# Kernel tuning notes

Hardware: AMD Instinct MI355X
Metric: run time of the kernel (lower is better)

Reference implementation:

```python
import jax, jax.numpy as jnp
import numpy as np
from jax import lax

# ConvTranspose2d(stride=1, padding=p) == conv with spatially-flipped, in/out-swapped
# weight and padding k-1-p per side. Here k=3, p=1 -> conv padding (1,1).
K = 3
P = 1
_CONV_PAD = K - 1 - P  # = 1

def _rconv(a, w):
    # a: [N,C,H,Wf] real, w: [O,I,kH,kW]
    return lax.conv_general_dilated(
        a, w, window_strides=(1, 1),
        padding=[(_CONV_PAD, _CONV_PAD), (_CONV_PAD, _CONV_PAD)],
        dimension_numbers=("NCHW", "OIHW", "NCHW"))


def setup_inputs() -> dict:
    key = jax.random.key(0)
    k1, k2, k3, k4, k5 = jax.random.split(key, 5)
    N, C_IN, C_OUT, H, W = 8, 16, 16, 512, 512
    x = jax.random.normal(k1, (N, C_IN, H, W), dtype=jnp.float32)
    # torch ConvTranspose2d weight layout: (in, out, kH, kW), complex64 split into re/im
    scale = 1.0 / np.sqrt(C_IN * K * K)
    w_real = jax.random.normal(k2, (C_IN, C_OUT, K, K), dtype=jnp.float32) * scale
    w_imag = jax.random.normal(k3, (C_IN, C_OUT, K, K), dtype=jnp.float32) * scale
    b_real = jax.random.normal(k4, (C_OUT,), dtype=jnp.float32) * scale
    b_imag = jax.random.normal(k5, (C_OUT,), dtype=jnp.float32) * scale
    return {"x": x, "w_real": w_real, "w_imag": w_imag, "b_real": b_real, "b_imag": b_imag}


def reference(x, w_real, w_imag, b_real, b_imag):
    # rfftn over last two dims (norm='backward')
    X = jnp.fft.rfftn(x, axes=(-2, -1), norm="backward")  # [N,C,H,W//2+1] complex64
    Xr, Xi = jnp.real(X), jnp.imag(X)
    # convert transpose-conv weight to equivalent conv weight: flip spatial, swap in/out
    wr = jnp.transpose(jnp.flip(w_real, axis=(-2, -1)), (1, 0, 2, 3))
    wi = jnp.transpose(jnp.flip(w_imag, axis=(-2, -1)), (1, 0, 2, 3))
    # complex conv via real/imag decomposition
    Yr = _rconv(Xr, wr) - _rconv(Xi, wi) + b_real[:, None, None]
    Yi = _rconv(Xr, wi) + _rconv(Xi, wr) + b_imag[:, None, None]
    Y = lax.complex(Yr, Yi)
    # irfftn with no explicit s: last dim -> 2*(Wf-1) = W
    return jnp.fft.irfftn(Y, axes=(-2, -1), norm="backward")
```

## Files before the change

### kernel.cpp

```cpp
#include <hip/hip_runtime.h>
#include <math.h>

#define PI_F 3.14159265358979323846f

#define FI(i) ((i) + ((i) >> 4))
#define CSTRIDE 544

__device__ inline float2 cmulf(float2 a, float2 b) {
    return make_float2(a.x * b.x - a.y * b.y, a.x * b.y + a.y * b.x);
}
__device__ inline float2 cadd(float2 a, float2 b) { return make_float2(a.x + b.x, a.y + b.y); }
__device__ inline float2 csub(float2 a, float2 b) { return make_float2(a.x - b.x, a.y - b.y); }

__device__ inline void cmac(float2& a, float2 w, float2 v) {
    a.x = fmaf(w.x, v.x, a.x);
    a.x = fmaf(-w.y, v.y, a.x);
    a.y = fmaf(w.x, v.y, a.y);
    a.y = fmaf(w.y, v.x, a.y);
}

__device__ inline int xcd_remap(int bid, int q) {
    return (bid & 7) * q + (bid >> 3);
}

__device__ inline void build_tbl128(float2* tbl, int tid) {
    if (tid < 128) {
        float ang = -2.0f * PI_F * (float)tid * (1.0f / 512.0f);
        tbl[tid] = make_float2(cosf(ang), sinf(ang));
    }
}

template <int NCOLS>
__device__ inline float2* fft512_r4(float2* a, float2* b, const float2* tbl, int tid, bool inv) {
    const int bf = tid & 127;
    const int cp = tid >> 7;
#pragma unroll
    for (int st = 0; st < 4; ++st) {
        const int slog = 2 * st;
        const int s = 1 << slog;
        const int p = bf >> slog;
        const int q = bf & (s - 1);
        float2 w1 = tbl[p << slog];
        if (inv) w1.y = -w1.y;
        const float2 w2 = cmulf(w1, w1);
        const float2 w3 = cmulf(w2, w1);
        const int i0 = bf;
        const int ob = q + (p << (slog + 2));
#pragma unroll
        for (int t = 0; t < NCOLS / 2; ++t) {
            const int cc = cp + 2 * t;
            const float2* ac = a + cc * CSTRIDE;
            float2* bc = b + cc * CSTRIDE;
            float2 A = ac[FI(i0)];
            float2 B = ac[FI(i0 + 128)];
            float2 C = ac[FI(i0 + 256)];
            float2 D = ac[FI(i0 + 384)];
            float2 apc = cadd(A, C), amc = csub(A, C);
            float2 bpd = cadd(B, D), bmd = csub(B, D);
            float2 jb = make_float2(-bmd.y, bmd.x);
            if (inv) { jb.x = -jb.x; jb.y = -jb.y; }
            bc[FI(ob)]           = cadd(apc, bpd);
            bc[FI(ob + s)]       = cmulf(csub(amc, jb), w1);
            bc[FI(ob + 2 * s)]   = cmulf(csub(apc, bpd), w2);
            bc[FI(ob + 3 * s)]   = cmulf(cadd(amc, jb), w3);
        }
        __syncthreads();
        float2* tmp = a; a = b; b = tmp;
    }
    {
#pragma unroll
        for (int cc = 0; cc < NCOLS; ++cc) {
            const float2* ac = a + cc * CSTRIDE;
            float2* bc = b + cc * CSTRIDE;
            float2 A = ac[FI(tid)];
            float2 B = ac[FI(tid + 256)];
            bc[FI(tid)]       = cadd(A, B);
            bc[FI(tid + 256)] = csub(A, B);
        }
        __syncthreads();
        float2* tmp = a; a = b; b = tmp;
    }
    return a;
}

__global__ __launch_bounds__(256) void k_row_rfft(const float* __restrict__ x,
                                                  float2* __restrict__ G) {
    __shared__ float2 b0[4 * CSTRIDE], b1[4 * CSTRIDE], tbl[128];
    int tid = threadIdx.x;
    int nc = blockIdx.x >> 7;
    int h0 = (blockIdx.x & 127) * 4;
    build_tbl128(tbl, tid);
    const float4* xr = (const float4*)(x + ((size_t)nc * 512 + h0) * 512);
#pragma unroll
    for (int j = 0; j < 2; ++j) {
        int t4 = tid + 256 * j;
        float4 v = xr[t4];
        int e = t4 * 4;
        int k = e >> 9, i = e & 511;
        float2* dst = b0 + k * CSTRIDE + FI(i);
        dst[0] = make_float2(v.x, 0.0f);
        dst[1] = make_float2(v.y, 0.0f);
        dst[2] = make_float2(v.z, 0.0f);
        dst[3] = make_float2(v.w, 0.0f);
    }
    __syncthreads();
    float2* res = fft512_r4<4>(b0, b1, tbl, tid, false);
#pragma unroll
    for (int k = 0; k < 4; ++k) {
        float2* g = G + ((size_t)(nc * 512 + h0 + k)) * 257;
        g[tid] = res[k * CSTRIDE + FI(tid)];
        if (tid == 0) g[256] = res[k * CSTRIDE + FI(256)];
    }
}

__global__ __launch_bounds__(256) void k_col_fft(const float2* __restrict__ G,
                                                 float2* __restrict__ XT) {
    __shared__ float2 b0[4 * CSTRIDE], b1[4 * CSTRIDE], tbl[128];
    int tid = threadIdx.x;
    int l = xcd_remap(blockIdx.x, 1040);
    int nc = l / 65;
    int v0 = (l % 65) * 4;
    build_tbl128(tbl, tid);
#pragma unroll
    for (int i = 0; i < 8; ++i) {
        int e = tid + 256 * i;
        int k = e & 3, h = e >> 2;
        int v = v0 + k;
        float2 val = make_float2(0.0f, 0.0f);
        if (v < 257) val = G[((size_t)nc * 512 + h) * 257 + v];
        b0[k * CSTRIDE + FI(h)] = val;
    }
    __syncthreads();
    float2* res = fft512_r4<4>(b0, b1, tbl, tid, false);
#pragma unroll
    for (int k = 0; k < 4; ++k) {
        int v = v0 + k;
        if (v < 257) {
            float2* dst = XT + ((size_t)nc * 257 + v) * 512;
            dst[tid]       = res[k * CSTRIDE + FI(tid)];
            dst[tid + 256] = res[k * CSTRIDE + FI(tid + 256)];
        }
    }
}

__global__ __launch_bounds__(256, 4) void k_conv(const float2* __restrict__ XT,
                                                 float2* __restrict__ YT,
                                                 const float* __restrict__ wr,
                                                 const float* __restrict__ wi,
                                                 const float* __restrict__ br,
                                                 const float* __restrict__ bi) {
    __shared__ float2 Xs[16 * 4 * 66];
    int tid = threadIdx.x;
    int bid = blockIdx.x;
    int ut = bid & 7;
    int rest = bid >> 3;
    int vt = rest % 129;
    int n = rest / 129;
    int u0 = ut * 64;
    int v0 = vt * 2;

    for (int l = tid; l < 4224; l += 256) {
        int c = l / 264;
        int rem = l - c * 264;
        int dvr = rem / 66;
        int uu = rem - dvr * 66;
        int vg = v0 - 1 + dvr;
        int ug = u0 - 1 + uu;
        float2 val = make_float2(0.0f, 0.0f);
        if (vg >= 0 && vg < 257 && ug >= 0 && ug < 512)
            val = XT[(((size_t)n * 16 + c) * 257 + vg) * 512 + ug];
        Xs[l] = val;
    }
    __syncthreads();

    int lane = tid & 63;
    int wv = __builtin_amdgcn_readfirstlane(tid >> 6);
    int o0 = wv * 4;

    float2 acc[2][4];
#pragma unroll
    for (int oo = 0; oo < 4; ++oo) {
        float2 bv = make_float2(br[o0 + oo], bi[o0 + oo]);
        acc[0][oo] = bv;
        acc[1][oo] = bv;
    }

    for (int c = 0; c < 16; ++c) {
        float2 xv[4][3];
#pragma unroll
        for (int dvr = 0; dvr < 4; ++dvr) {
            const float2* row = &Xs[(c * 4 + dvr) * 66];
            xv[dvr][0] = row[lane];
            xv[dvr][1] = row[lane + 1];
            xv[dvr][2] = row[lane + 2];
        }
#pragma unroll
        for (int oo = 0; oo < 4; ++oo) {
            const float* wrp = wr + ((size_t)(c * 16 + o0 + oo)) * 9;
            const float* wip = wi + ((size_t)(c * 16 + o0 + oo)) * 9;
            float wre[9], wim[9];
#pragma unroll
            for (int t = 0; t < 9; ++t) { wre[t] = wrp[t]; wim[t] = wip[t]; }
#pragma unroll
            for (int kw = 0; kw < 3; ++kw) {
#pragma unroll
                for (int kh = 0; kh < 3; ++kh) {
                    int t = kh * 3 + kw;
                    int xj = 2 - kh;
                    float2 w = make_float2(wre[t], wim[t]);
                    cmac(acc[0][oo], w, xv[2 - kw][xj]);
                    cmac(acc[1][oo], w, xv[3 - kw][xj]);
                }
            }
        }
    }

#pragma unroll
    for (int oo = 0; oo < 4; ++oo) {
#pragma unroll
        for (int vv = 0; vv < 2; ++vv) {
            int v = v0 + vv;
            if (v < 257)
                YT[(((size_t)n * 16 + o0 + oo) * 257 + v) * 512 + u0 + lane] =
                    acc[vv][oo];
        }
    }
}

__global__ __launch_bounds__(256) void k_col_ifft(const float2* __restrict__ YT,
                                                  float2* __restrict__ ZT) {
    __shared__ float2 b0[4 * CSTRIDE], b1[4 * CSTRIDE], tbl[128];
    int tid = threadIdx.x;
    int no = blockIdx.x / 65;
    int v0 = (blockIdx.x % 65) * 4;
    build_tbl128(tbl, tid);
#pragma unroll
    for (int k = 0; k < 4; ++k) {
        int v = v0 + k;
        const float2* src = YT + ((size_t)no * 257 + (v < 257 ? v : 256)) * 512;
        b0[k * CSTRIDE + FI(tid)]       = src[tid];
        b0[k * CSTRIDE + FI(tid + 256)] = src[tid + 256];
    }
    __syncthreads();
    float2* res = fft512_r4<4>(b0, b1, tbl, tid, true);
    const float sc = 1.0f / 512.0f;
#pragma unroll
    for (int k = 0; k < 4; ++k) {
        int v = v0 + k;
        if (v < 257) {
            float2* dst = ZT + ((size_t)no * 257 + v) * 512;
            float2 r0 = res[k * CSTRIDE + FI(tid)];
            float2 r1 = res[k * CSTRIDE + FI(tid + 256)];
            dst[tid]       = make_float2(r0.x * sc, r0.y * sc);
            dst[tid + 256] = make_float2(r1.x * sc, r1.y * sc);
        }
    }
}

__global__ __launch_bounds__(256) void k_row_irfft(const float2* __restrict__ ZT,
                                                   float* __restrict__ out) {
    __shared__ float2 b0[4 * CSTRIDE], b1[4 * CSTRIDE], tbl[128];
    int tid = threadIdx.x;
    int l = xcd_remap(blockIdx.x, 2048);
    int no = l >> 7;
    int h0 = (l & 127) * 4;
    build_tbl128(tbl, tid);
#pragma unroll
    for (int i = 0; i < 5; ++i) {
        int e = tid + 256 * i;
        if (e < 1028) {
            int k = e & 3, vv = e >> 2;
            float2 val = ZT[((size_t)no * 257 + vv) * 512 + h0 + k];
            if (vv == 0 || vv == 256) val.y = 0.0f;
            b0[k * CSTRIDE + FI(vv)] = val;
        }
    }
    __syncthreads();
#pragma unroll
    for (int i = 0; i < 4; ++i) {
        int e = tid + 256 * i;
        if (e < 1020) {
            int k = e & 3, vv = 257 + (e >> 2);
            float2 s = b0[k * CSTRIDE + FI(512 - vv)];
            b0[k * CSTRIDE + FI(vv)] = make_float2(s.x, -s.y);
        }
    }
    __syncthreads();
    float2* res = fft512_r4<4>(b0, b1, tbl, tid, true);
    const float sc = 1.0f / 512.0f;
#pragma unroll
    for (int k = 0; k < 4; ++k) {
        float* dst = out + ((size_t)no * 512 + h0 + k) * 512;
        dst[tid]       = res[k * CSTRIDE + FI(tid)].x * sc;
        dst[tid + 256] = res[k * CSTRIDE + FI(tid + 256)].x * sc;
    }
}

extern "C" void kernel_launch(void* const* d_in, const int* in_sizes, int n_in,
                              void* d_out, int out_size, void* d_ws, size_t ws_size,
                              hipStream_t stream) {
    const float* x  = (const float*)d_in[0];
    const float* wr = (const float*)d_in[1];
    const float* wi = (const float*)d_in[2];
    const float* br = (const float*)d_in[3];
    const float* bi = (const float*)d_in[4];
    float* out = (float*)d_out;

    const size_t bufElems = (size_t)128 * 257 * 512;
    float2* A = (float2*)d_ws;
    float2* B = A + bufElems;

    k_row_rfft<<<128 * 128, 256, 0, stream>>>(x, A);
    k_col_fft<<<128 * 65, 256, 0, stream>>>(A, B);
    k_conv<<<8 * 129 * 8, 256, 0, stream>>>(B, A, wr, wi, br, bi);
    k_col_ifft<<<128 * 65, 256, 0, stream>>>(A, B);
    k_row_irfft<<<128 * 128, 256, 0, stream>>>(B, out);
}
```

Measured before the change: 674.6 us.

## Replace block-wide radix-4 FFT with per-wave register radix-8 FFT

Replaces the shared-memory radix-4 FFT, which used five block-wide barriers and a twiddle table, with a per-wavefront 512-point FFT. Each lane holds 8 values in registers and runs three radix-8 stages with two LDS transposes between them. Wave-local fences replace __syncthreads, and twiddles come from sincosf instead of a table. This is meant to cut barrier stalls and LDS traffic. In exchange it adds transcendental math and more register pressure, and the column kernels now do strided, uncoalesced global loads per lane. The Hermitian extension in the irfft row kernel now reads ZT directly instead of mirroring in LDS.

New measurement: 697.5 us. +3.4%, slower.

```diff
diff --git a/kernel.cpp b/kernel.cpp
--- a/kernel.cpp
+++ b/kernel.cpp
@@ -1,10 +1,7 @@
 #include <hip/hip_runtime.h>
 #include <math.h>
 
-#define PI_F 3.14159265358979323846f
-
 #define FI(i) ((i) + ((i) >> 4))
-#define CSTRIDE 544
 
 __device__ inline float2 cmulf(float2 a, float2 b) {
     return make_float2(a.x * b.x - a.y * b.y, a.x * b.y + a.y * b.x);
@@ -23,124 +20,116 @@
     return (bid & 7) * q + (bid >> 3);
 }
 
-__device__ inline void build_tbl128(float2* tbl, int tid) {
-    if (tid < 128) {
-        float ang = -2.0f * PI_F * (float)tid * (1.0f / 512.0f);
-        tbl[tid] = make_float2(cosf(ang), sinf(ang));
-    }
-}
-
-template <int NCOLS>
-__device__ inline float2* fft512_r4(float2* a, float2* b, const float2* tbl, int tid, bool inv) {
-    const int bf = tid & 127;
-    const int cp = tid >> 7;
-#pragma unroll
-    for (int st = 0; st < 4; ++st) {
-        const int slog = 2 * st;
-        const int s = 1 << slog;
-        const int p = bf >> slog;
-        const int q = bf & (s - 1);
-        float2 w1 = tbl[p << slog];
-        if (inv) w1.y = -w1.y;
-        const float2 w2 = cmulf(w1, w1);
-        const float2 w3 = cmulf(w2, w1);
-        const int i0 = bf;
-        const int ob = q + (p << (slog + 2));
-#pragma unroll
-        for (int t = 0; t < NCOLS / 2; ++t) {
-            const int cc = cp + 2 * t;
-            const float2* ac = a + cc * CSTRIDE;
-            float2* bc = b + cc * CSTRIDE;
-            float2 A = ac[FI(i0)];
-            float2 B = ac[FI(i0 + 128)];
-            float2 C = ac[FI(i0 + 256)];
-            float2 D = ac[FI(i0 + 384)];
-            float2 apc = cadd(A, C), amc = csub(A, C);
-            float2 bpd = cadd(B, D), bmd = csub(B, D);
-            float2 jb = make_float2(-bmd.y, bmd.x);
-            if (inv) { jb.x = -jb.x; jb.y = -jb.y; }
-            bc[FI(ob)]           = cadd(apc, bpd);
-            bc[FI(ob + s)]       = cmulf(csub(amc, jb), w1);
-            bc[FI(ob + 2 * s)]   = cmulf(csub(apc, bpd), w2);
-            bc[FI(ob + 3 * s)]   = cmulf(cadd(amc, jb), w3);
-        }
-        __syncthreads();
-        float2* tmp = a; a = b; b = tmp;
-    }
+__device__ inline void wave_fence() {
+    asm volatile("s_waitcnt lgkmcnt(0)" ::: "memory");
+    __builtin_amdgcn_sched_barrier(0);
+}
+
+template <bool INV>
+__device__ inline float2 rot90(float2 z) {
+    return INV ? make_float2(-z.y, z.x) : make_float2(z.y, -z.x);
+}
+
+template <bool INV>
+__device__ inline void dft8(float2 v[8]) {
+    const float R2 = 0.70710678118654752f;
+    float2 t0 = cadd(v[0], v[4]), t1 = csub(v[0], v[4]);
+    float2 t2 = cadd(v[2], v[6]), t3 = csub(v[2], v[6]);
+    float2 s0 = cadd(v[1], v[5]), s1 = csub(v[1], v[5]);
+    float2 s2 = cadd(v[3], v[7]), s3 = csub(v[3], v[7]);
+    float2 rt3 = rot90<INV>(t3), rs3 = rot90<INV>(s3);
+    float2 E0 = cadd(t0, t2), E1 = cadd(t1, rt3), E2 = csub(t0, t2), E3 = csub(t1, rt3);
+    float2 O0 = cadd(s0, s2), O1 = cadd(s1, rs3), O2 = csub(s0, s2), O3 = csub(s1, rs3);
+    float2 rO1 = rot90<INV>(O1), rO2 = rot90<INV>(O2), rO3 = rot90<INV>(O3);
+    float2 a1 = make_float2(R2 * (O1.x + rO1.x), R2 * (O1.y + rO1.y));
+    float2 a2 = rO2;
+    float2 a3 = make_float2(R2 * (rO3.x - O3.x), R2 * (rO3.y - O3.y));
+    v[0] = cadd(E0, O0); v[4] = csub(E0, O0);
+    v[1] = cadd(E1, a1); v[5] = csub(E1, a1);
+    v[2] = cadd(E2, a2); v[6] = csub(E2, a2);
+    v[3] = cadd(E3, a3); v[7] = csub(E3, a3);
+}
+
+__device__ inline void twiddle8(float2 v[8], float2 w1) {
+    float2 w2 = cmulf(w1, w1);
+    float2 w3 = cmulf(w2, w1);
+    float2 w4 = cmulf(w2, w2);
+    float2 w5 = cmulf(w4, w1);
+    float2 w6 = cmulf(w3, w3);
+    float2 w7 = cmulf(w4, w3);
+    v[1] = cmulf(v[1], w1); v[2] = cmulf(v[2], w2); v[3] = cmulf(v[3], w3);
+    v[4] = cmulf(v[4], w4); v[5] = cmulf(v[5], w5); v[6] = cmulf(v[6], w6);
+    v[7] = cmulf(v[7], w7);
+}
+
+template <bool INV>
+__device__ inline void fft512_wave(float2 v[8], float2* bufA, float2* bufB, int lane) {
+    const float sg = INV ? (6.2831853071795865f / 512.0f)
+                         : (-6.2831853071795865f / 512.0f);
+    dft8<INV>(v);
     {
-#pragma unroll
-        for (int cc = 0; cc < NCOLS; ++cc) {
-            const float2* ac = a + cc * CSTRIDE;
-            float2* bc = b + cc * CSTRIDE;
-            float2 A = ac[FI(tid)];
-            float2 B = ac[FI(tid + 256)];
-            bc[FI(tid)]       = cadd(A, B);
-            bc[FI(tid + 256)] = csub(A, B);
-        }
-        __syncthreads();
-        float2* tmp = a; a = b; b = tmp;
-    }
-    return a;
+        float ang = sg * (float)lane;
+        float2 w1;
+        sincosf(ang, &w1.y, &w1.x);
+        twiddle8(v, w1);
+    }
+#pragma unroll
+    for (int m = 0; m < 8; ++m) bufA[FI(8 * lane + m)] = v[m];
+    wave_fence();
+#pragma unroll
+    for (int j = 0; j < 8; ++j) v[j] = bufA[FI(lane + 64 * j)];
+    dft8<INV>(v);
+    {
+        float ang = sg * (float)(lane & 56);
+        float2 w1;
+        sincosf(ang, &w1.y, &w1.x);
+        twiddle8(v, w1);
+    }
+    {
+        int ob = (lane & 7) + ((lane >> 3) << 6);
+#pragma unroll
+        for (int m = 0; m < 8; ++m) bufB[FI(ob + 8 * m)] = v[m];
+    }
+    wave_fence();
+#pragma unroll
+    for (int j = 0; j < 8; ++j) v[j] = bufB[FI(lane + 64 * j)];
+    dft8<INV>(v);
 }
 
 __global__ __launch_bounds__(256) void k_row_rfft(const float* __restrict__ x,
                                                   float2* __restrict__ G) {
-    __shared__ float2 b0[4 * CSTRIDE], b1[4 * CSTRIDE], tbl[128];
-    int tid = threadIdx.x;
-    int nc = blockIdx.x >> 7;
-    int h0 = (blockIdx.x & 127) * 4;
-    build_tbl128(tbl, tid);
-    const float4* xr = (const float4*)(x + ((size_t)nc * 512 + h0) * 512);
-#pragma unroll
-    for (int j = 0; j < 2; ++j) {
-        int t4 = tid + 256 * j;
-        float4 v = xr[t4];
-        int e = t4 * 4;
-        int k = e >> 9, i = e & 511;
-        float2* dst = b0 + k * CSTRIDE + FI(i);
-        dst[0] = make_float2(v.x, 0.0f);
-        dst[1] = make_float2(v.y, 0.0f);
-        dst[2] = make_float2(v.z, 0.0f);
-        dst[3] = make_float2(v.w, 0.0f);
-    }
-    __syncthreads();
-    float2* res = fft512_r4<4>(b0, b1, tbl, tid, false);
-#pragma unroll
-    for (int k = 0; k < 4; ++k) {
-        float2* g = G + ((size_t)(nc * 512 + h0 + k)) * 257;
-        g[tid] = res[k * CSTRIDE + FI(tid)];
-        if (tid == 0) g[256] = res[k * CSTRIDE + FI(256)];
-    }
+    __shared__ float2 lds[4][2][544];
+    int lane = threadIdx.x & 63;
+    int w = threadIdx.x >> 6;
+    int row = blockIdx.x * 4 + w;
+    const float* xr = x + (size_t)row * 512;
+    float2 v[8];
+#pragma unroll
+    for (int j = 0; j < 8; ++j) v[j] = make_float2(xr[lane + 64 * j], 0.0f);
+    fft512_wave<false>(v, lds[w][0], lds[w][1], lane);
+    float2* g = G + (size_t)row * 257;
+#pragma unroll
+    for (int m = 0; m < 4; ++m) g[lane + 64 * m] = v[m];
+    if (lane == 0) g[256] = v[4];
 }
 
 __global__ __launch_bounds__(256) void k_col_fft(const float2* __restrict__ G,
                                                  float2* __restrict__ XT) {
-    __shared__ float2 b0[4 * CSTRIDE], b1[4 * CSTRIDE], tbl[128];
-    int tid = threadIdx.x;
+    __shared__ float2 lds[4][2][544];
+    int lane = threadIdx.x & 63;
+    int w = threadIdx.x >> 6;
     int l = xcd_remap(blockIdx.x, 1040);
     int nc = l / 65;
-    int v0 = (l % 65) * 4;
-    build_tbl128(tbl, tid);
-#pragma unroll
-    for (int i = 0; i < 8; ++i) {
-        int e = tid + 256 * i;
-        int k = e & 3, h = e >> 2;
-        int v = v0 + k;
-        float2 val = make_float2(0.0f, 0.0f);
-        if (v < 257) val = G[((size_t)nc * 512 + h) * 257 + v];
-        b0[k * CSTRIDE + FI(h)] = val;
-    }
-    __syncthreads();
-    float2* res = fft512_r4<4>(b0, b1, tbl, tid, false);
-#pragma unroll
-    for (int k = 0; k < 4; ++k) {
-        int v = v0 + k;
-        if (v < 257) {
-            float2* dst = XT + ((size_t)nc * 257 + v) * 512;
-            dst[tid]       = res[k * CSTRIDE + FI(tid)];
-            dst[tid + 256] = res[k * CSTRIDE + FI(tid + 256)];
-        }
-    }
+    int v = (l % 65) * 4 + w;
+    if (v >= 257) return;
+    float2 vv[8];
+#pragma unroll
+    for (int j = 0; j < 8; ++j)
+        vv[j] = G[((size_t)nc * 512 + lane + 64 * j) * 257 + v];
+    fft512_wave<false>(vv, lds[w][0], lds[w][1], lane);
+    float2* dst = XT + ((size_t)nc * 257 + v) * 512;
+#pragma unroll
+    for (int m = 0; m < 8; ++m) dst[lane + 64 * m] = vv[m];
 }
 
 __global__ __launch_bounds__(256, 4) void k_conv(const float2* __restrict__ XT,
@@ -229,71 +218,51 @@
 
 __global__ __launch_bounds__(256) void k_col_ifft(const float2* __restrict__ YT,
                                                   float2* __restrict__ ZT) {
-    __shared__ float2 b0[4 * CSTRIDE], b1[4 * CSTRIDE], tbl[128];
-    int tid = threadIdx.x;
+    __shared__ float2 lds[4][2][544];
+    int lane = threadIdx.x & 63;
+    int w = threadIdx.x >> 6;
     int no = blockIdx.x / 65;
-    int v0 = (blockIdx.x % 65) * 4;
-    build_tbl128(tbl, tid);
-#pragma unroll
-    for (int k = 0; k < 4; ++k) {
-        int v = v0 + k;
-        const float2* src = YT + ((size_t)no * 257 + (v < 257 ? v : 256)) * 512;
-        b0[k * CSTRIDE + FI(tid)]       = src[tid];
-        b0[k * CSTRIDE + FI(tid + 256)] = src[tid + 256];
-    }
-    __syncthreads();
-    float2* res = fft512_r4<4>(b0, b1, tbl, tid, true);
+    int v = (blockIdx.x % 65) * 4 + w;
+    if (v >= 257) return;
+    const float2* src = YT + ((size_t)no * 257 + v) * 512;
+    float2 vv[8];
+#pragma unroll
+    for (int j = 0; j < 8; ++j) vv[j] = src[lane + 64 * j];
+    fft512_wave<true>(vv, lds[w][0], lds[w][1], lane);
     const float sc = 1.0f / 512.0f;
-#pragma unroll
-    for (int k = 0; k < 4; ++k) {
-        int v = v0 + k;
-        if (v < 257) {
-            float2* dst = ZT + ((size_t)no * 257 + v) * 512;
-            float2 r0 = res[k * CSTRIDE + FI(tid)];
-            float2 r1 = res[k * CSTRIDE + FI(tid + 256)];
-            dst[tid]       = make_float2(r0.x * sc, r0.y * sc);
-            dst[tid + 256] = make_float2(r1.x * sc, r1.y * sc);
-        }
-    }
+    float2* dst = ZT + ((size_t)no * 257 + v) * 512;
+#pragma unroll
+    for (int m = 0; m < 8; ++m)
+        dst[lane + 64 * m] = make_float2(vv[m].x * sc, vv[m].y * sc);
 }
 
 __global__ __launch_bounds__(256) void k_row_irfft(const float2* __restrict__ ZT,
                                                    float* __restrict__ out) {
-    __shared__ float2 b0[4 * CSTRIDE], b1[4 * CSTRIDE], tbl[128];
-    int tid = threadIdx.x;
+    __shared__ float2 lds[4][2][544];
+    int lane = threadIdx.x & 63;
+    int w = threadIdx.x >> 6;
     int l = xcd_remap(blockIdx.x, 2048);
     int no = l >> 7;
-    int h0 = (l & 127) * 4;
-    build_tbl128(tbl, tid);
-#pragma unroll
-    for (int i = 0; i < 5; ++i) {
-        int e = tid + 256 * i;
-        if (e < 1028) {
-            int k = e & 3, vv = e >> 2;
-            float2 val = ZT[((size_t)no * 257 + vv) * 512 + h0 + k];
-            if (vv == 0 || vv == 256) val.y = 0.0f;
-            b0[k * CSTRIDE + FI(vv)] = val;
-        }
-    }
-    __syncthreads();
-#pragma unroll
-    for (int i = 0; i < 4; ++i) {
-        int e = tid + 256 * i;
-        if (e < 1020) {
-            int k = e & 3, vv = 257 + (e >> 2);
-            float2 s = b0[k * CSTRIDE + FI(512 - vv)];
-            b0[k * CSTRIDE + FI(vv)] = make_float2(s.x, -s.y);
-        }
-    }
-    __syncthreads();
-    float2* res = fft512_r4<4>(b0, b1, tbl, tid, true);
+    int h = (l & 127) * 4 + w;
+    float2 v[8];
+#pragma unroll
+    for (int j = 0; j < 8; ++j) {
+        int i = lane + 64 * j;
+        float2 val;
+        if (i <= 256) {
+            val = ZT[((size_t)no * 257 + i) * 512 + h];
+            if (i == 0 || i == 256) val.y = 0.0f;
+        } else {
+            val = ZT[((size_t)no * 257 + (512 - i)) * 512 + h];
+            val.y = -val.y;
+        }
+        v[j] = val;
+    }
+    fft512_wave<true>(v, lds[w][0], lds[w][1], lane);
     const float sc = 1.0f / 512.0f;
-#pragma unroll
-    for (int k = 0; k < 4; ++k) {
-        float* dst = out + ((size_t)no * 512 + h0 + k) * 512;
-        dst[tid]       = res[k * CSTRIDE + FI(tid)].x * sc;
-        dst[tid + 256] = res[k * CSTRIDE + FI(tid + 256)].x * sc;
-    }
+    float* dst = out + ((size_t)no * 512 + h) * 512;
+#pragma unroll
+    for (int m = 0; m < 8; ++m) dst[lane + 64 * m] = v[m].x * sc;
 }
 
 extern "C" void kernel_launch(void* const* d_in, const int* in_sizes, int n_in,
@@ -310,9 +279,9 @@
     float2* A = (float2*)d_ws;
     float2* B = A + bufElems;
 
-    k_row_rfft<<<128 * 128, 256, 0, stream>>>(x, A);
+    k_row_rfft<<<16384, 256, 0, stream>>>(x, A);
     k_col_fft<<<128 * 65, 256, 0, stream>>>(A, B);
     k_conv<<<8 * 129 * 8, 256, 0, stream>>>(B, A, wr, wi, br, bi);
     k_col_ifft<<<128 * 65, 256, 0, stream>>>(A, B);
-    k_row_irfft<<<128 * 128, 256, 0, stream>>>(B, out);
-}
+    k_row_irfft<<<16384, 256, 0, stream>>>(B, out);
+}
```

## Use per-wave register radix-8 FFT512 in column FFT and row IRFFT

Applied to the files above, without the earlier changes.

Replaces the block-wide radix-4 shared-memory FFT in k_col_fft and k_row_irfft with a per-wavefront radix-8 FFT that keeps 8 values per lane in registers. The data goes through shared memory only at the two transposes, and those use wave-level lgkmcnt fences instead of block barriers. Twiddles come from __sincosf and shuffles rather than a table. Blocks now hold 1024 threads covering 16 transforms, each wave doing one, and row_irfft builds the Hermitian extension during the register load. The aim is to cut block-wide syncs, the table builds and shared-memory passes, at the cost of larger blocks, more registers per lane and slightly less accurate fast sincos.

Result: faster. 637.6 us (-5.5%).

```diff
diff --git a/kernel.cpp b/kernel.cpp
--- a/kernel.cpp
+++ b/kernel.cpp
@@ -5,6 +5,7 @@
 
 #define FI(i) ((i) + ((i) >> 4))
 #define CSTRIDE 544
+#define TSTRIDE 546
 
 __device__ inline float2 cmulf(float2 a, float2 b) {
     return make_float2(a.x * b.x - a.y * b.y, a.x * b.y + a.y * b.x);
@@ -83,6 +84,77 @@
     return a;
 }
 
+__device__ inline void wave_fence() {
+    asm volatile("s_waitcnt lgkmcnt(0)" ::: "memory");
+    __builtin_amdgcn_sched_barrier(0);
+}
+
+template <bool INV>
+__device__ inline float2 rot90(float2 z) {
+    return INV ? make_float2(-z.y, z.x) : make_float2(z.y, -z.x);
+}
+
+template <bool INV>
+__device__ inline void dft8(float2 v[8]) {
+    const float R2 = 0.70710678118654752f;
+    float2 t0 = cadd(v[0], v[4]), t1 = csub(v[0], v[4]);
+    float2 t2 = cadd(v[2], v[6]), t3 = csub(v[2], v[6]);
+    float2 s0 = cadd(v[1], v[5]), s1 = csub(v[1], v[5]);
+    float2 s2 = cadd(v[3], v[7]), s3 = csub(v[3], v[7]);
+    float2 rt3 = rot90<INV>(t3), rs3 = rot90<INV>(s3);
+    float2 E0 = cadd(t0, t2), E1 = cadd(t1, rt3), E2 = csub(t0, t2), E3 = csub(t1, rt3);
+    float2 O0 = cadd(s0, s2), O1 = cadd(s1, rs3), O2 = csub(s0, s2), O3 = csub(s1, rs3);
+    float2 rO1 = rot90<INV>(O1), rO2 = rot90<INV>(O2), rO3 = rot90<INV>(O3);
+    float2 a1 = make_float2(R2 * (O1.x + rO1.x), R2 * (O1.y + rO1.y));
+    float2 a2 = rO2;
+    float2 a3 = make_float2(R2 * (rO3.x - O3.x), R2 * (rO3.y - O3.y));
+    v[0] = cadd(E0, O0); v[4] = csub(E0, O0);
+    v[1] = cadd(E1, a1); v[5] = csub(E1, a1);
+    v[2] = cadd(E2, a2); v[6] = csub(E2, a2);
+    v[3] = cadd(E3, a3); v[7] = csub(E3, a3);
+}
+
+__device__ inline void twiddle8(float2 v[8], float2 w1) {
+    float2 w2 = cmulf(w1, w1);
+    float2 w3 = cmulf(w2, w1);
+    float2 w4 = cmulf(w2, w2);
+    float2 w5 = cmulf(w4, w1);
+    float2 w6 = cmulf(w3, w3);
+    float2 w7 = cmulf(w4, w3);
+    v[1] = cmulf(v[1], w1); v[2] = cmulf(v[2], w2); v[3] = cmulf(v[3], w3);
+    v[4] = cmulf(v[4], w4); v[5] = cmulf(v[5], w5); v[6] = cmulf(v[6], w6);
+    v[7] = cmulf(v[7], w7);
+}
+
+template <bool INV>
+__device__ inline void fft512_wave_ip(float2 v[8], float2* R, int lane) {
+    const float sg = INV ? (6.2831853071795865f / 512.0f)
+                         : (-6.2831853071795865f / 512.0f);
+    float2 w1;
+    __sincosf(sg * (float)lane, &w1.y, &w1.x);
+    dft8<INV>(v);
+    twiddle8(v, w1);
+#pragma unroll
+    for (int m = 0; m < 8; ++m) R[FI(8 * lane + m)] = v[m];
+    wave_fence();
+#pragma unroll
+    for (int j = 0; j < 8; ++j) v[j] = R[FI(lane + 64 * j)];
+    float2 w1b;
+    w1b.x = __shfl(w1.x, lane & 56);
+    w1b.y = __shfl(w1.y, lane & 56);
+    dft8<INV>(v);
+    twiddle8(v, w1b);
+    {
+        int ob = (lane & 7) + ((lane >> 3) << 6);
+#pragma unroll
+        for (int m = 0; m < 8; ++m) R[FI(ob + 8 * m)] = v[m];
+    }
+    wave_fence();
+#pragma unroll
+    for (int j = 0; j < 8; ++j) v[j] = R[FI(lane + 64 * j)];
+    dft8<INV>(v);
+}
+
 __global__ __launch_bounds__(256) void k_row_rfft(const float* __restrict__ x,
                                                   float2* __restrict__ G) {
     __shared__ float2 b0[4 * CSTRIDE], b1[4 * CSTRIDE], tbl[128];
@@ -113,33 +185,34 @@
     }
 }
 
-__global__ __launch_bounds__(256) void k_col_fft(const float2* __restrict__ G,
-                                                 float2* __restrict__ XT) {
-    __shared__ float2 b0[4 * CSTRIDE], b1[4 * CSTRIDE], tbl[128];
-    int tid = threadIdx.x;
-    int l = xcd_remap(blockIdx.x, 1040);
-    int nc = l / 65;
-    int v0 = (l % 65) * 4;
-    build_tbl128(tbl, tid);
-#pragma unroll
-    for (int i = 0; i < 8; ++i) {
-        int e = tid + 256 * i;
-        int k = e & 3, h = e >> 2;
-        int v = v0 + k;
+__global__ __launch_bounds__(1024) void k_col_fft(const float2* __restrict__ G,
+                                                  float2* __restrict__ XT) {
+    __shared__ float2 tile[16][TSTRIDE];
+    int tid = threadIdx.x;
+    int l = xcd_remap(blockIdx.x, 272);
+    int nc = l / 17;
+    int v0 = (l % 17) * 16;
+#pragma unroll
+    for (int j = 0; j < 8; ++j) {
+        int e = tid + 1024 * j;
+        int dv = e & 15, h = e >> 4;
+        int v = v0 + dv;
         float2 val = make_float2(0.0f, 0.0f);
         if (v < 257) val = G[((size_t)nc * 512 + h) * 257 + v];
-        b0[k * CSTRIDE + FI(h)] = val;
-    }
-    __syncthreads();
-    float2* res = fft512_r4<4>(b0, b1, tbl, tid, false);
-#pragma unroll
-    for (int k = 0; k < 4; ++k) {
-        int v = v0 + k;
-        if (v < 257) {
-            float2* dst = XT + ((size_t)nc * 257 + v) * 512;
-            dst[tid]       = res[k * CSTRIDE + FI(tid)];
-            dst[tid + 256] = res[k * CSTRIDE + FI(tid + 256)];
-        }
+        tile[dv][FI(h)] = val;
+    }
+    __syncthreads();
+    int lane = tid & 63, w = tid >> 6;
+    float2* R = tile[w];
+    float2 vv[8];
+#pragma unroll
+    for (int j = 0; j < 8; ++j) vv[j] = R[FI(lane + 64 * j)];
+    fft512_wave_ip<false>(vv, R, lane);
+    int v = v0 + w;
+    if (v < 257) {
+        float2* dst = XT + ((size_t)nc * 257 + v) * 512;
+#pragma unroll
+        for (int m = 0; m < 8; ++m) dst[lane + 64 * m] = vv[m];
     }
 }
 
@@ -257,43 +330,42 @@
     }
 }
 
-__global__ __launch_bounds__(256) void k_row_irfft(const float2* __restrict__ ZT,
-                                                   float* __restrict__ out) {
-    __shared__ float2 b0[4 * CSTRIDE], b1[4 * CSTRIDE], tbl[128];
-    int tid = threadIdx.x;
-    int l = xcd_remap(blockIdx.x, 2048);
-    int no = l >> 7;
-    int h0 = (l & 127) * 4;
-    build_tbl128(tbl, tid);
-#pragma unroll
-    for (int i = 0; i < 5; ++i) {
-        int e = tid + 256 * i;
-        if (e < 1028) {
-            int k = e & 3, vv = e >> 2;
-            float2 val = ZT[((size_t)no * 257 + vv) * 512 + h0 + k];
-            if (vv == 0 || vv == 256) val.y = 0.0f;
-            b0[k * CSTRIDE + FI(vv)] = val;
-        }
-    }
-    __syncthreads();
-#pragma unroll
-    for (int i = 0; i < 4; ++i) {
-        int e = tid + 256 * i;
-        if (e < 1020) {
-            int k = e & 3, vv = 257 + (e >> 2);
-            float2 s = b0[k * CSTRIDE + FI(512 - vv)];
-            b0[k * CSTRIDE + FI(vv)] = make_float2(s.x, -s.y);
-        }
-    }
-    __syncthreads();
-    float2* res = fft512_r4<4>(b0, b1, tbl, tid, true);
+__global__ __launch_bounds__(1024) void k_row_irfft(const float2* __restrict__ ZT,
+                                                    float* __restrict__ out) {
+    __shared__ float2 tile[16][TSTRIDE];
+    int tid = threadIdx.x;
+    int no = blockIdx.x >> 5;
+    int h0 = (blockIdx.x & 31) * 16;
+#pragma unroll
+    for (int j = 0; j < 5; ++j) {
+        int e = tid + 1024 * j;
+        if (e < 4112) {
+            int dh = e & 15, vv = e >> 4;
+            tile[dh][FI(vv)] = ZT[((size_t)no * 257 + vv) * 512 + h0 + dh];
+        }
+    }
+    __syncthreads();
+    int lane = tid & 63, w = tid >> 6;
+    float2* R = tile[w];
+    float2 v[8];
+#pragma unroll
+    for (int j = 0; j < 8; ++j) {
+        int i = lane + 64 * j;
+        float2 val;
+        if (i <= 256) {
+            val = R[FI(i)];
+            if (i == 0 || i == 256) val.y = 0.0f;
+        } else {
+            val = R[FI(512 - i)];
+            val.y = -val.y;
+        }
+        v[j] = val;
+    }
+    fft512_wave_ip<true>(v, R, lane);
     const float sc = 1.0f / 512.0f;
-#pragma unroll
-    for (int k = 0; k < 4; ++k) {
-        float* dst = out + ((size_t)no * 512 + h0 + k) * 512;
-        dst[tid]       = res[k * CSTRIDE + FI(tid)].x * sc;
-        dst[tid + 256] = res[k * CSTRIDE + FI(tid + 256)].x * sc;
-    }
+    float* dst = out + ((size_t)no * 512 + h0 + w) * 512;
+#pragma unroll
+    for (int m = 0; m < 8; ++m) dst[lane + 64 * m] = v[m].x * sc;
 }
 
 extern "C" void kernel_launch(void* const* d_in, const int* in_sizes, int n_in,
@@ -311,8 +383,8 @@
     float2* B = A + bufElems;
 
     k_row_rfft<<<128 * 128, 256, 0, stream>>>(x, A);
-    k_col_fft<<<128 * 65, 256, 0, stream>>>(A, B);
+    k_col_fft<<<128 * 17, 1024, 0, stream>>>(A, B);
     k_conv<<<8 * 129 * 8, 256, 0, stream>>>(B, A, wr, wi, br, bi);
     k_col_ifft<<<128 * 65, 256, 0, stream>>>(A, B);
-    k_row_irfft<<<128 * 128, 256, 0, stream>>>(B, out);
-}
+    k_row_irfft<<<128 * 32, 1024, 0, stream>>>(B, out);
+}
```
